# Kernel tuning notes

Measured on AMD Instinct MI355X. Metric: run time of the kernel, lower is better.

Reference implementation:

```python
import jax, jax.numpy as jnp
import numpy as np

B, L, D, H, DFF, C = 16, 1024, 256, 4, 2048, 3
NS, NC = 4, 4
DH = D // H


def _ln(x, g, b):
    m = x.mean(-1, keepdims=True)
    v = ((x - m) ** 2).mean(-1, keepdims=True)
    return (x - m) / jnp.sqrt(v + 1e-5) * g + b


def setup_inputs() -> dict:
    key = jax.random.key(0)
    ks = jax.random.split(key, 24)
    n = lambda k, s: jax.random.normal(k, s, jnp.float32) * 0.02
    return {
        'shape_idxs': jax.random.randint(ks[0], (B, L), 0, NS, jnp.int32),
        'color_idxs': jax.random.randint(ks[1], (B, L), 0, NC, jnp.int32),
        'shape_emb': n(ks[2], (NS, D)),
        'color_emb': n(ks[3], (NC, D)),
        'Wq': n(ks[4], (D, D)), 'bq': jnp.zeros((D,)),
        'Wk': n(ks[5], (D, D)), 'bk': jnp.zeros((D,)),
        'Wv': n(ks[6], (D, D)), 'bv': jnp.zeros((D,)),
        'Wo': n(ks[7], (D, D)), 'bo': jnp.zeros((D,)),
        'g1': jnp.ones((D,)), 'be1': jnp.zeros((D,)),
        'W1': n(ks[8], (D, DFF)), 'bf1': jnp.zeros((DFF,)),
        'W2': n(ks[9], (DFF, D)), 'bf2': jnp.zeros((D,)),
        'g2': jnp.ones((D,)), 'be2': jnp.zeros((D,)),
        'Wl': n(ks[10], (D, C)), 'bl': jnp.zeros((C,)),
        'Wp1': n(ks[11], (D, D)), 'bp1': jnp.zeros((D,)),
        'Wp2': n(ks[12], (D, 1)), 'bp2': jnp.zeros((1,)),
        'wc': n(ks[13], (1, 1)), 'bc': jnp.zeros((1,)),
    }


def reference(shape_idxs, color_idxs, shape_emb, color_emb, Wq, bq, Wk, bk, Wv, bv,
              Wo, bo, g1, be1, W1, bf1, W2, bf2, g2, be2, Wl, bl,
              Wp1, bp1, Wp2, bp2, wc, bc):
    # embed (dropout is identity in eval)
    x = shape_emb[shape_idxs] + color_emb[color_idxs]  # [B,L,D]
    # post-norm transformer encoder layer (PyTorch default)
    heads = lambda t: t.reshape(B, L, H, DH)
    q, k, v = heads(x @ Wq + bq), heads(x @ Wk + bk), heads(x @ Wv + bv)
    scores = jnp.einsum('blhd,bmhd->bhlm', q, k) / jnp.sqrt(jnp.float32(DH))
    attn = jax.nn.softmax(scores, axis=-1)
    ctx = jnp.einsum('bhlm,bmhd->blhd', attn, v).reshape(B, L, D)
    y = _ln(x + ctx @ Wo + bo, g1, be1)
    ff = jax.nn.relu(y @ W1 + bf1) @ W2 + bf2
    y = _ln(y + ff, g2, be2)  # trans_out [B,L,D]
    # latent logits / KL(prior || probs) with batchmean reduction
    logits = y @ Wl + bl
    logp = jax.nn.log_softmax(logits, axis=-1)
    prior = 1.0 / C
    kl_loss = jnp.sum(prior * (jnp.log(jnp.float32(prior)) - logp)) / B
    # data-dependent boundary segmentation (argmax of probs == argmax of logits)
    boundaries = (jnp.argmax(logits, axis=-1) == 0)
    boundaries = boundaries.at[:, 0].set(True)
    closed = boundaries & (jnp.arange(L) > 0)  # closure at l>0 ends segment at l
    seg_id = jnp.cumsum(closed.astype(jnp.int32), axis=1) - closed  # exclusive cumsum
    gid = (jnp.arange(B)[:, None] * L + seg_id).reshape(-1)  # global segment ids
    sums = jax.ops.segment_sum(y.reshape(B * L, D), gid, num_segments=B * L)
    counts = jax.ops.segment_sum(jnp.ones((B * L,), jnp.float32), gid, num_segments=B * L)
    means = sums / jnp.maximum(counts, 1.0)[:, None]  # per-segment mean [B*L,D]
    # predicate net + composition, mean over valid segments
    preds = jax.nn.sigmoid(jax.nn.relu(means @ Wp1 + bp1) @ Wp2 + bp2)  # [B*L,1]
    comp = (preds * wc[0, 0] + bc[0]).reshape(B, L)
    valid = (counts > 0).reshape(B, L).astype(jnp.float32)
    mean_comp = jnp.sum(comp * valid, axis=1) / jnp.sum(valid, axis=1)
    final_scores = jax.nn.sigmoid(mean_comp)
    return final_scores, kl_loss
```

## Files before the change

### kernel.cpp

```cpp
#include <hip/hip_runtime.h>


typedef unsigned short u16;
typedef u16    u16x4  __attribute__((ext_vector_type(4)));
typedef u16    u16x8  __attribute__((ext_vector_type(8)));
typedef __bf16 bf16x8 __attribute__((ext_vector_type(8)));
typedef float  f32x4  __attribute__((ext_vector_type(4)));

__device__ __forceinline__ float bf2f(u16 u) {
    union { unsigned int i; float f; } v; v.i = ((unsigned int)u) << 16; return v.f;
}
__device__ __forceinline__ u16 f2bf(float f) {
    union { float f; unsigned int i; } v; v.f = f;
    unsigned int r = (v.i + 0x7FFFu + ((v.i >> 16) & 1u)) >> 16;
    return (u16)r;
}
__device__ __forceinline__ u16 f2bf_fast(float f) {
    union { __bf16 h; u16 u; } v; v.h = (__bf16)f; return v.u;
}
__device__ __forceinline__ void gll16(const u16* g, u16* l) {
    __builtin_amdgcn_global_load_lds((__attribute__((address_space(1))) void*)(u16*)g,
                                     (__attribute__((address_space(3))) void*)l, 16, 0, 0);
}
__device__ __forceinline__ int get_mode(const int* __restrict__ detp) {
    int s = 0;
#pragma unroll 8
    for (int i = 0; i < 64; ++i) s += detp[i];
    return s > 16;
}

__global__ __launch_bounds__(256) void k_detect(const u16* __restrict__ w1raw,
                                                int* __restrict__ detp) {
    int i = blockIdx.x * 256 + threadIdx.x;
    int bad = 0;
    for (int k = i; k < 65536; k += 64 * 256) {
        unsigned v = w1raw[k] & 0x7FFFu;
        if (v >= 0x7F80u) bad++;
    }
    for (int off = 32; off >= 1; off >>= 1) bad += __shfl_xor(bad, off);
    __shared__ int bs[4];
    if ((threadIdx.x & 63) == 0) bs[threadIdx.x >> 6] = bad;
    __syncthreads();
    if (threadIdx.x == 0) detp[blockIdx.x] = bs[0] + bs[1] + bs[2] + bs[3];
}
__global__ void k_sentinel_f32(float* __restrict__ out, int code) {
    int t = threadIdx.x;
    if (t < 17) out[t] = (float)code;
}

struct PrepTab {
    const void* src[7];
    u16*        dst[7];
    int         K[7], N[7];
    float       scale[7];
    int         tstart[8];
    const void* isrc[17];
    unsigned    idstoff[17];
    int         in[17];
    float       iscale[17];
    u16*        ing;
};
__global__ __launch_bounds__(256) void k_prep(PrepTab tt, const int* __restrict__ detp) {
    int m = get_mode(detp);
    int bx = blockIdx.x;
    if (bx >= tt.tstart[7]) {
        int t = bx - tt.tstart[7];
        int n = tt.in[t];
        float sc = tt.iscale[t];
        u16* dst = tt.ing + tt.idstoff[t];
        for (int i = threadIdx.x; i < n; i += 256) {
            float v = m ? ((const float*)tt.isrc[t])[i] : bf2f(((const u16*)tt.isrc[t])[i]);
            dst[i] = f2bf(v * sc);
        }
        return;
    }
    __shared__ u16 tile[32][33];
    int wgt = 0;
#pragma unroll
    for (int i = 1; i < 7; ++i) if (bx >= tt.tstart[i]) wgt = i;
    int local = bx - tt.tstart[wgt];
    int K = tt.K[wgt], N = tt.N[wgt];
    float sc = tt.scale[wgt];
    int ntx = N >> 5;
    int txt = local % ntx, tyt = local / ntx;
    const void* W = tt.src[wgt];
    u16* Wt = tt.dst[wgt];
    int tx = threadIdx.x & 31, ty = threadIdx.x >> 5;
    int n = txt * 32 + tx;
    for (int i = ty; i < 32; i += 8) {
        size_t idx = (size_t)(tyt * 32 + i) * N + n;
        float v = m ? ((const float*)W)[idx] : bf2f(((const u16*)W)[idx]);
        tile[i][tx] = f2bf(v * sc);
    }
    __syncthreads();
    int k2 = tyt * 32 + tx;
    for (int i = ty; i < 32; i += 8) {
        int n2 = txt * 32 + i;
        Wt[(size_t)n2 * K + k2] = tile[tx][i];
    }
}

__global__ __launch_bounds__(256) void k_embed(const int* __restrict__ si,
                                               const int* __restrict__ ci,
                                               const void* __restrict__ se,
                                               const void* __restrict__ ce,
                                               u16* __restrict__ X,
                                               const int* __restrict__ detp) {
    int m = get_mode(detp);
    int t = blockIdx.x * 256 + threadIdx.x;
    int row = t >> 5, seg = (t & 31) * 8;
    int s = si[row], c = ci[row];
    u16x8 o;
    if (m) {
        const float* sp = (const float*)se + s * 256 + seg;
        const float* cp = (const float*)ce + c * 256 + seg;
#pragma unroll
        for (int e = 0; e < 8; ++e) o[e] = f2bf(sp[e] + cp[e]);
    } else {
        u16x8 a = *(const u16x8*)((const u16*)se + s * 256 + seg);
        u16x8 b = *(const u16x8*)((const u16*)ce + c * 256 + seg);
#pragma unroll
        for (int e = 0; e < 8; ++e) o[e] = f2bf(bf2f(a[e]) + bf2f(b[e]));
    }
    *(u16x8*)&X[(size_t)row * 256 + seg] = o;
}

__global__ __launch_bounds__(256) void k_gemm_bt(const u16* __restrict__ A,
                                                 const u16* __restrict__ Bt,
                                                 const u16* __restrict__ bias,
                                                 u16* __restrict__ C,
                                                 int N, int K, int relu, int gx) {
    __shared__ u16 As[128][32];
    __shared__ u16 Bs[128][32];
    const int tid = threadIdx.x;
    const int xcd = blockIdx.x & 7, j = blockIdx.x >> 3;
    const int m0 = (xcd * 16 + j / gx) * 128, n0 = (j % gx) * 128;
    const int lane = tid & 63, wid = tid >> 6;
    const int wm = (wid & 1) * 64, wn = (wid >> 1) * 64;
    const int m16 = lane & 15, quad = lane >> 4;
    f32x4 acc[4][4] = {};
    const int arow = tid >> 2;
    const int ac8  = (tid & 3) * 8;
    const u16* Ap0 = A  + (size_t)(m0 + arow) * K + ac8;
    const u16* Ap1 = A  + (size_t)(m0 + 64 + arow) * K + ac8;
    const u16* Bp0 = Bt + (size_t)(n0 + arow) * K + ac8;
    const u16* Bp1 = Bt + (size_t)(n0 + 64 + arow) * K + ac8;
    u16* lA0 = &As[arow][ac8];
    u16* lA1 = &As[64 + arow][ac8];
    u16* lB0 = &Bs[arow][ac8];
    u16* lB1 = &Bs[64 + arow][ac8];

    for (int k0 = 0; k0 < K; k0 += 32) {
        __syncthreads();
        gll16(Ap0 + k0, lA0);
        gll16(Ap1 + k0, lA1);
        gll16(Bp0 + k0, lB0);
        gll16(Bp1 + k0, lB1);
        __syncthreads();
        bf16x8 af[4], bfv[4];
#pragma unroll
        for (int i = 0; i < 4; ++i)
            af[i] = *(const bf16x8*)&As[wm + i * 16 + m16][quad * 8];
#pragma unroll
        for (int j2 = 0; j2 < 4; ++j2)
            bfv[j2] = *(const bf16x8*)&Bs[wn + j2 * 16 + m16][quad * 8];
#pragma unroll
        for (int i = 0; i < 4; ++i)
#pragma unroll
            for (int j2 = 0; j2 < 4; ++j2)
                acc[i][j2] = __builtin_amdgcn_mfma_f32_16x16x32_bf16(
                    af[i], bfv[j2], acc[i][j2], 0, 0, 0);
    }

#pragma unroll
    for (int i = 0; i < 4; ++i) {
        int row = m0 + wm + i * 16 + quad * 4;
#pragma unroll
        for (int j2 = 0; j2 < 4; ++j2) {
            int col = n0 + wn + j2 * 16 + m16;
            float bv = bf2f(bias[col]);
#pragma unroll
            for (int r = 0; r < 4; ++r) {
                float v = acc[i][j2][r] + bv;
                if (relu) v = fmaxf(v, 0.f);
                C[(size_t)(row + r) * N + col] = f2bf_fast(v);
            }
        }
    }
}

__global__ __launch_bounds__(256) void k_gemm64(const u16* __restrict__ A,
                                                const u16* __restrict__ Bt,
                                                const u16* __restrict__ bias,
                                                u16* __restrict__ C,
                                                int N, int K, int relu,
                                                int gx, int mtpx,
                                                u16* __restrict__ vt) {
    __shared__ u16 As0[64][32], As1[64][32];
    __shared__ u16 Bs0[128][32], Bs1[128][32];
    const int tid = threadIdx.x;
    const int xcd = blockIdx.x & 7, j = blockIdx.x >> 3;
    const int m0 = (xcd * mtpx + j / gx) * 64, n0 = (j % gx) * 128;
    const int vmode = (vt != nullptr) && (n0 >= 512);
    const int lane = tid & 63, wid = tid >> 6;
    const int wm = (wid & 1) * 32, wn = (wid >> 1) * 64;
    const int m16 = lane & 15, quad = lane >> 4;
    f32x4 acc[2][4] = {};
    const int arow = tid >> 2;
    const int ac8  = (tid & 3) * 8;
    const u16* Ap  = A  + (size_t)(m0 + arow) * K + ac8;
    const u16* Bp0 = Bt + (size_t)(n0 + arow) * K + ac8;
    const u16* Bp1 = Bt + (size_t)(n0 + 64 + arow) * K + ac8;
    u16* lA0  = &As0[arow][ac8];
    u16* lA1  = &As1[arow][ac8];
    u16* lB00 = &Bs0[arow][ac8];
    u16* lB01 = &Bs0[64 + arow][ac8];
    u16* lB10 = &Bs1[arow][ac8];
    u16* lB11 = &Bs1[64 + arow][ac8];

    for (int k0 = 0; k0 < K; k0 += 64) {
        __syncthreads();
        gll16(Ap + k0,        lA0);
        gll16(Ap + k0 + 32,   lA1);
        gll16(Bp0 + k0,       lB00);
        gll16(Bp0 + k0 + 32,  lB10);
        gll16(Bp1 + k0,       lB01);
        gll16(Bp1 + k0 + 32,  lB11);
        __syncthreads();
#pragma unroll
        for (int ks = 0; ks < 2; ++ks) {
            bf16x8 af[2], bfv[4];
#pragma unroll
            for (int i = 0; i < 2; ++i)
                af[i] = ks == 0 ? *(const bf16x8*)&As0[wm + i * 16 + m16][quad * 8]
                                : *(const bf16x8*)&As1[wm + i * 16 + m16][quad * 8];
#pragma unroll
            for (int j2 = 0; j2 < 4; ++j2)
                bfv[j2] = ks == 0 ? *(const bf16x8*)&Bs0[wn + j2 * 16 + m16][quad * 8]
                                  : *(const bf16x8*)&Bs1[wn + j2 * 16 + m16][quad * 8];
#pragma unroll
            for (int i = 0; i < 2; ++i)
#pragma unroll
                for (int j2 = 0; j2 < 4; ++j2)
                    acc[i][j2] = __builtin_amdgcn_mfma_f32_16x16x32_bf16(
                        af[i], bfv[j2], acc[i][j2], 0, 0, 0);
        }
    }

#pragma unroll
    for (int i = 0; i < 2; ++i) {
        int row = m0 + wm + i * 16 + quad * 4;
#pragma unroll
        for (int j2 = 0; j2 < 4; ++j2) {
            int col = n0 + wn + j2 * 16 + m16;
            float bv = bf2f(bias[col]);
            if (vmode) {
                int ch = col - 512;
                u16x4 o;
#pragma unroll
                for (int r = 0; r < 4; ++r) o[r] = f2bf_fast(acc[i][j2][r] + bv);
                size_t vb = ((size_t)((row >> 10) * 4 + (ch >> 6)) * 64 + (ch & 63)) * 1024
                          + (row & 1023);
                *(u16x4*)&vt[vb] = o;
            } else {
#pragma unroll
                for (int r = 0; r < 4; ++r) {
                    float v = acc[i][j2][r] + bv;
                    if (relu) v = fmaxf(v, 0.f);
                    C[(size_t)(row + r) * N + col] = f2bf_fast(v);
                }
            }
        }
    }
}

__global__ __launch_bounds__(256) void k_gemm64n(const u16* __restrict__ A,
                                                 const u16* __restrict__ Bt,
                                                 const u16* __restrict__ bias,
                                                 u16* __restrict__ C,
                                                 int N, int K, int relu,
                                                 int gnx, int mtpx,
                                                 const float* __restrict__ gate) {
    __shared__ u16 As0[64][32], As1[64][32];
    __shared__ u16 Bs0[64][32], Bs1[64][32];
    const int tid = threadIdx.x;
    const int xcd = blockIdx.x & 7, j = blockIdx.x >> 3;
    const int m0 = (xcd * mtpx + j / gnx) * 64, n0 = (j % gnx) * 64;
    if (gate && gate[m0] == 0.f) return;
    const int lane = tid & 63, w = tid >> 6;
    const int m16 = lane & 15, quad = lane >> 4;
    f32x4 acc[4] = {};
    const int arow = tid >> 2;
    const int ac8  = (tid & 3) * 8;
    const u16* Ap = A  + (size_t)(m0 + arow) * K + ac8;
    const u16* Bp = Bt + (size_t)(n0 + arow) * K + ac8;
    u16* lA0 = &As0[arow][ac8];
    u16* lA1 = &As1[arow][ac8];
    u16* lB0 = &Bs0[arow][ac8];
    u16* lB1 = &Bs1[arow][ac8];

    for (int k0 = 0; k0 < K; k0 += 64) {
        __syncthreads();
        gll16(Ap + k0,       lA0);
        gll16(Ap + k0 + 32,  lA1);
        gll16(Bp + k0,       lB0);
        gll16(Bp + k0 + 32,  lB1);
        __syncthreads();
#pragma unroll
        for (int ks = 0; ks < 2; ++ks) {
            bf16x8 af = ks == 0 ? *(const bf16x8*)&As0[w * 16 + m16][quad * 8]
                                : *(const bf16x8*)&As1[w * 16 + m16][quad * 8];
#pragma unroll
            for (int nt = 0; nt < 4; ++nt) {
                bf16x8 bfv = ks == 0 ? *(const bf16x8*)&Bs0[nt * 16 + m16][quad * 8]
                                     : *(const bf16x8*)&Bs1[nt * 16 + m16][quad * 8];
                acc[nt] = __builtin_amdgcn_mfma_f32_16x16x32_bf16(af, bfv, acc[nt], 0, 0, 0);
            }
        }
    }

#pragma unroll
    for (int nt = 0; nt < 4; ++nt) {
        int col = n0 + nt * 16 + m16;
        float bv = bf2f(bias[col]);
        int row = m0 + w * 16 + quad * 4;
#pragma unroll
        for (int r = 0; r < 4; ++r) {
            float v = acc[nt][r] + bv;
            if (relu) v = fmaxf(v, 0.f);
            C[(size_t)(row + r) * N + col] = f2bf_fast(v);
        }
    }
}

__global__ __launch_bounds__(256) void k_attn_mfma(const u16* __restrict__ QKV,
                                                   const u16* __restrict__ VT,
                                                   u16* __restrict__ CTX) {
    __shared__ u16 Ks[64][72];
    __shared__ u16 Vts[64][72];
    const int tid = threadIdx.x, lane = tid & 63, w = tid >> 6;
    const int quad = lane >> 4, c = lane & 15;
    const int blk = blockIdx.x;
    const int xcd = blk & 7, local = blk >> 3;
    const int bh = xcd * 8 + (local >> 4);
    const int qt = local & 15;
    const int b = bh >> 2, h = bh & 3;
    const int qrow0 = b * 1024 + qt * 64;

    const u16* qptr = QKV + (size_t)(qrow0 + w * 16 + c) * 768 + h * 64;
    bf16x8 aq0 = *(const bf16x8*)(qptr + quad * 8);
    bf16x8 aq1 = *(const bf16x8*)(qptr + 32 + quad * 8);

    bf16x8 ones;
    {
        union { u16 u; __bf16 h; } v; v.u = 0x3F80;
#pragma unroll
        for (int e = 0; e < 8; ++e) ones[e] = v.h;
    }

    f32x4 acc_o[4] = {};
    f32x4 acc_l = {};

    const u16* kbase  = QKV + (size_t)(b * 1024) * 768 + 256 + h * 64;
    const u16* vtbase = VT + (size_t)(bh * 64) * 1024;
    const int skk = tid >> 3, sc8 = (tid & 7) * 8;
    const int swk = (skk & ~12) | ((skk & 4) << 1) | ((skk & 8) >> 1);
    const int sra = ((c & 8) << 1) | (c & 4) | (c & 3);

    for (int t = 0; t < 16; ++t) {
        __syncthreads();
#pragma unroll
        for (int it = 0; it < 2; ++it) {
            int rr = skk + 32 * it;
            *(u16x8*)&Ks[swk + 32 * it][sc8] =
                *(const u16x8*)(kbase + (size_t)(t * 64 + rr) * 768 + sc8);
            *(u16x8*)&Vts[rr][sc8] = *(const u16x8*)(vtbase + (size_t)rr * 1024 + t * 64 + sc8);
        }
        __syncthreads();

#pragma unroll
        for (int ks = 0; ks < 2; ++ks) {
            const int ra = ks * 32 + sra;
            bf16x8 ka0 = *(const bf16x8*)&Ks[ra][quad * 8];
            bf16x8 ka1 = *(const bf16x8*)&Ks[ra][32 + quad * 8];
            bf16x8 kb0 = *(const bf16x8*)&Ks[ra + 8][quad * 8];
            bf16x8 kb1 = *(const bf16x8*)&Ks[ra + 8][32 + quad * 8];
            f32x4 za = {}, zb = {};
            za = __builtin_amdgcn_mfma_f32_16x16x32_bf16(ka0, aq0, za, 0, 0, 0);
            za = __builtin_amdgcn_mfma_f32_16x16x32_bf16(ka1, aq1, za, 0, 0, 0);
            zb = __builtin_amdgcn_mfma_f32_16x16x32_bf16(kb0, aq0, zb, 0, 0, 0);
            zb = __builtin_amdgcn_mfma_f32_16x16x32_bf16(kb1, aq1, zb, 0, 0, 0);

            bf16x8 ap;
#pragma unroll
            for (int r = 0; r < 4; ++r) {
                ap[r]     = (__bf16)exp2f(fminf(za[r], 80.f));
                ap[4 + r] = (__bf16)exp2f(fminf(zb[r], 80.f));
            }

            acc_l = __builtin_amdgcn_mfma_f32_16x16x32_bf16(ap, ones, acc_l, 0, 0, 0);
#pragma unroll
            for (int nt = 0; nt < 4; ++nt) {
                bf16x8 bv = *(const bf16x8*)&Vts[nt * 16 + c][ks * 32 + quad * 8];
                acc_o[nt] = __builtin_amdgcn_mfma_f32_16x16x32_bf16(ap, bv, acc_o[nt], 0, 0, 0);
            }
        }
    }

#pragma unroll
    for (int nt = 0; nt < 4; ++nt) {
        int col = h * 64 + nt * 16 + c;
#pragma unroll
        for (int r = 0; r < 4; ++r) {
            int row = qrow0 + w * 16 + quad * 4 + r;
            CTX[(size_t)row * 256 + col] = f2bf_fast(acc_o[nt][r] / acc_l[r]);
        }
    }
}

__global__ __launch_bounds__(256) void k_ln(const u16* __restrict__ A,
                                            const u16* __restrict__ R,
                                            const u16* __restrict__ g,
                                            const u16* __restrict__ be,
                                            u16* __restrict__ out) {
    int w = threadIdx.x >> 6, lane = threadIdx.x & 63;
    int row = blockIdx.x * 4 + w;
    size_t base = (size_t)row * 256 + lane * 4;
    u16x4 a4 = *(const u16x4*)&A[base];
    u16x4 r4 = *(const u16x4*)&R[base];
    float v[4];
    float s = 0.f, sq = 0.f;
#pragma unroll
    for (int j = 0; j < 4; ++j) {
        v[j] = bf2f(a4[j]) + bf2f(r4[j]);
        s += v[j]; sq += v[j] * v[j];
    }
    for (int off = 32; off >= 1; off >>= 1) { s += __shfl_xor(s, off); sq += __shfl_xor(sq, off); }
    float mean = s * (1.f / 256.f);
    float var  = sq * (1.f / 256.f) - mean * mean;
    float rs   = rsqrtf(var + 1e-5f);
    u16x4 o;
#pragma unroll
    for (int j = 0; j < 4; ++j) {
        int d = lane * 4 + j;
        o[j] = f2bf((v[j] - mean) * rs * bf2f(g[d]) + bf2f(be[d]));
    }
    *(u16x4*)&out[base] = o;
}

__global__ __launch_bounds__(256) void k_logits(const u16* __restrict__ FFO,
                                                const u16* __restrict__ Y1,
                                                const u16* __restrict__ g2,
                                                const u16* __restrict__ be2,
                                                const u16* __restrict__ Wl,
                                                const u16* __restrict__ bl,
                                                u16* __restrict__ Y2,
                                                float* __restrict__ klpart,
                                                int* __restrict__ flags) {
    const int tid = threadIdx.x, lane = tid & 63, w = tid >> 6;
    float wv[4][3], gv[4], bev[4];
#pragma unroll
    for (int j = 0; j < 4; ++j) {
        int d = lane * 4 + j;
        gv[j]  = bf2f(g2[d]);
        bev[j] = bf2f(be2[d]);
#pragma unroll
        for (int c = 0; c < 3; ++c) wv[j][c] = bf2f(Wl[d * 3 + c]);
    }
    const float b0 = bf2f(bl[0]), b1 = bf2f(bl[1]), b2 = bf2f(bl[2]);
    float klsum = 0.f;
    const int row0 = blockIdx.x * 16 + w * 4;
    for (int i = 0; i < 4; ++i) {
        int row = row0 + i;
        size_t base = (size_t)row * 256 + lane * 4;
        u16x4 f4 = *(const u16x4*)&FFO[base];
        u16x4 y4 = *(const u16x4*)&Y1[base];
        float v[4];
        float s = 0.f, sq = 0.f;
#pragma unroll
        for (int j = 0; j < 4; ++j) {
            v[j] = bf2f(f4[j]) + bf2f(y4[j]);
            s += v[j]; sq += v[j] * v[j];
        }
        for (int off = 32; off >= 1; off >>= 1) { s += __shfl_xor(s, off); sq += __shfl_xor(sq, off); }
        float mean = s * (1.f / 256.f);
        float var  = sq * (1.f / 256.f) - mean * mean;
        float rs   = rsqrtf(var + 1e-5f);
        u16x4 o;
        float a0 = 0.f, a1 = 0.f, a2 = 0.f;
#pragma unroll
        for (int j = 0; j < 4; ++j) {
            float yn = (v[j] - mean) * rs * gv[j] + bev[j];
            o[j] = f2bf(yn);
            float y = bf2f(o[j]);
            a0 += y * wv[j][0]; a1 += y * wv[j][1]; a2 += y * wv[j][2];
        }
        *(u16x4*)&Y2[base] = o;
        for (int off = 32; off >= 1; off >>= 1) {
            a0 += __shfl_xor(a0, off); a1 += __shfl_xor(a1, off); a2 += __shfl_xor(a2, off);
        }
        if (lane == 0) {
            float l0 = a0 + b0, l1 = a1 + b1, l2 = a2 + b2;
            float mx = fmaxf(l0, fmaxf(l1, l2));
            float lse = mx + __logf(__expf(l0 - mx) + __expf(l1 - mx) + __expf(l2 - mx));
            klsum += lse - (l0 + l1 + l2) * (1.f / 3.f) - 1.0986122886681098f;
            int am = 0; float bv = l0;
            if (l1 > bv) { bv = l1; am = 1; }
            if (l2 > bv) { am = 2; }
            int l = row & 1023;
            flags[row] = (am == 0 && l != 0) ? 1 : 0;
        }
    }
    __shared__ float kls[4];
    if (lane == 0) kls[w] = klsum;
    __syncthreads();
    if (tid == 0) klpart[blockIdx.x] = kls[0] + kls[1] + kls[2] + kls[3];
}

__global__ void k_scan(const int* __restrict__ flags, int* __restrict__ seg) {
    __shared__ int wsum[16];
    int b = blockIdx.x, t = threadIdx.x;
    int lane = t & 63, w = t >> 6;
    int f = flags[b * 1024 + t];
    int x = f;
#pragma unroll
    for (int off = 1; off < 64; off <<= 1) {
        int v = __shfl_up(x, off);
        if (lane >= off) x += v;
    }
    if (lane == 63) wsum[w] = x;
    __syncthreads();
    if (w == 0) {
        int s = (lane < 16) ? wsum[lane] : 0;
#pragma unroll
        for (int off = 1; off < 16; off <<= 1) {
            int v = __shfl_up(s, off);
            if (lane >= off) s += v;
        }
        if (lane < 16) wsum[lane] = s;
    }
    __syncthreads();
    int prefix = (w > 0) ? wsum[w - 1] : 0;
    seg[b * 1024 + t] = prefix + x - f;
}

__global__ __launch_bounds__(64) void k_segmean(const u16* __restrict__ Y,
                                                const int* __restrict__ seg,
                                                u16* __restrict__ means,
                                                float* __restrict__ cnt) {
    int g = blockIdx.x, lane = threadIdx.x;
    int b = g >> 10, s = g & 1023;
    const int* sb = seg + b * 1024;
    int target = s + (lane & 1);
    int lo = 0, hi = 1024;
    while (lo < hi) {
        int mid = (lo + hi) >> 1;
        if (sb[mid] < target) lo = mid + 1; else hi = mid;
    }
    int start = __shfl(lo, 0);
    int end   = __shfl(lo, 1);
    int n = end - start;
    if (lane == 0) cnt[g] = (float)n;
    if (n <= 0) return;
    f32x4 acc = {};
    for (int row = start; row < end; ++row) {
        u16x4 y4 = *(const u16x4*)&Y[(size_t)(b * 1024 + row) * 256 + lane * 4];
        acc[0] += bf2f(y4[0]); acc[1] += bf2f(y4[1]);
        acc[2] += bf2f(y4[2]); acc[3] += bf2f(y4[3]);
    }
    float inv = 1.f / (float)n;
    u16x4 o;
#pragma unroll
    for (int j = 0; j < 4; ++j) o[j] = f2bf(acc[j] * inv);
    *(u16x4*)&means[(size_t)g * 256 + lane * 4] = o;
}

__global__ __launch_bounds__(256) void k_preds(const u16* __restrict__ T,
                                               const u16* __restrict__ Wp2,
                                               const u16* __restrict__ bp2,
                                               const u16* __restrict__ wc,
                                               const u16* __restrict__ bc,
                                               const float* __restrict__ cnt,
                                               float* __restrict__ predp) {
    const int tid = threadIdx.x, lane = tid & 63, w = tid >> 6;
    float lwp[4];
#pragma unroll
    for (int j = 0; j < 4; ++j) lwp[j] = bf2f(Wp2[lane * 4 + j]);
    const float fb = bf2f(bp2[0]), fw = bf2f(wc[0]), fc = bf2f(bc[0]);
    float csum = 0.f, vsum = 0.f;
    const int g0 = blockIdx.x * 16 + w * 4;
    if (cnt[g0] != 0.f) {
        for (int i = 0; i < 4; ++i) {
            int g = g0 + i;
            u16x4 t4 = *(const u16x4*)&T[(size_t)g * 256 + lane * 4];
            float a = 0.f;
#pragma unroll
            for (int j = 0; j < 4; ++j) a += bf2f(t4[j]) * lwp[j];
            for (int off = 32; off >= 1; off >>= 1) a += __shfl_xor(a, off);
            if (lane == 0 && cnt[g] > 0.f) {
                float pred = 1.f / (1.f + __expf(-(a + fb)));
                csum += pred * fw + fc;
                vsum += 1.f;
            }
        }
    }
    __shared__ float cs[4], vs[4];
    if (lane == 0) { cs[w] = csum; vs[w] = vsum; }
    __syncthreads();
    if (tid == 0) {
        predp[2 * blockIdx.x]     = cs[0] + cs[1] + cs[2] + cs[3];
        predp[2 * blockIdx.x + 1] = vs[0] + vs[1] + vs[2] + vs[3];
    }
}

__global__ void k_final(const float* __restrict__ predp, const float* __restrict__ klp,
                        const int* __restrict__ detp, void* __restrict__ outv) {
    int t = threadIdx.x;
    float k = 0.f;
    for (int i = t; i < 1024; i += 64) k += klp[i];
    for (int off = 32; off >= 1; off >>= 1) k += __shfl_xor(k, off);
    float ktot = __shfl(k, 0);
    int batch = t >> 2, ch = t & 3;
    float c = 0.f, v = 0.f;
    for (int i = 0; i < 16; ++i) {
        int blk = batch * 64 + ch * 16 + i;
        c += predp[2 * blk];
        v += predp[2 * blk + 1];
    }
    c += __shfl_xor(c, 1); c += __shfl_xor(c, 2);
    v += __shfl_xor(v, 1); v += __shfl_xor(v, 2);
    int mode = get_mode(detp);
    if ((t & 3) == 0) {
        float d = v, nm = c;
        if (!(d > 0.f)) d = 1.f;
        if (isnan(nm) || isinf(nm)) nm = 0.f;
        float val = 1.f / (1.f + __expf(-nm / d));
        if (mode) ((float*)outv)[batch] = val;
        else      ((u16*)outv)[batch]   = f2bf(val);
    }
    if (t == 1) {
        float val = ktot * (1.f / 16.f);
        if (isnan(val) || isinf(val)) val = 0.f;
        if (mode) ((float*)outv)[16] = val;
        else      ((u16*)outv)[16]   = f2bf(val);
    }
}

extern "C" void kernel_launch(void* const* d_in, const int* in_sizes, int n_in,
                              void* d_out, int out_size, void* d_ws, size_t ws_size,
                              hipStream_t stream) {
    const int* shape_idxs = (const int*)d_in[0];
    const int* color_idxs = (const int*)d_in[1];
    char* ws = (char*)d_ws;
    const size_t MB = 1024 * 1024;

    if (ws_size < 90 * MB) {
        int wsMB = (int)(ws_size >> 20); if (wsMB > 250) wsMB = 250;
        k_sentinel_f32<<<1, 32, 0, stream>>>((float*)d_out, 200 + wsMB);
        return;
    }

    u16*   X     = (u16*)(ws);
    u16*   QKVb  = (u16*)(ws + 8 * MB);
    u16*   VT    = (u16*)(ws + 32 * MB);
    u16*   CTX   = (u16*)(ws + 40 * MB);
    u16*   CTXP  = (u16*)(ws + 48 * MB);
    u16*   Y1    = (u16*)(ws + 64 * MB);
    u16*   Hb    = (u16*)(ws);
    u16*   FFO   = (u16*)(ws + 72 * MB);
    u16*   Y2    = (u16*)(ws);
    u16*   MEANS = (u16*)(ws + 24 * MB);
    u16*   TB    = (u16*)(ws + 32 * MB);
    int*   FLAGS = (int*)(ws + 80 * MB);
    int*   SEG   = (int*)(ws + 80 * MB + 65536);
    float* CNT   = (float*)(ws + 80 * MB + 131072);
    float* KLP   = (float*)(ws + 80 * MB + 262144);
    float* PREDP = (float*)(ws + 80 * MB + 327680);
    u16*   W3T   = (u16*)(ws + 81 * MB);
    u16*   WoT   = (u16*)(ws + 81 * MB + 786432);
    u16*   Wp1T  = (u16*)(ws + 81 * MB + 917504);
    u16*   W1T   = (u16*)(ws + 82 * MB);
    u16*   W2T   = (u16*)(ws + 83 * MB);
    int*   DETP  = (int*)(ws + 84 * MB);
    u16*   ING   = (u16*)(ws + 85 * MB);

    const float QSCALE = 0.125f * 1.44269504f;

    PrepTab tt;
    const void* tsrc[7] = {d_in[4], d_in[6], d_in[8], d_in[10], d_in[22], d_in[14], d_in[16]};
    u16* tdst[7] = {W3T, W3T + 256 * 256, W3T + 512 * 256, WoT, Wp1T, W1T, W2T};
    int tK[7] = {256, 256, 256, 256, 256, 256, 2048};
    int tN[7] = {256, 256, 256, 256, 256, 2048, 256};
    int ts = 0;
    for (int i = 0; i < 7; ++i) {
        tt.src[i] = tsrc[i]; tt.dst[i] = tdst[i]; tt.K[i] = tK[i]; tt.N[i] = tN[i];
        tt.scale[i] = (i == 0) ? QSCALE : 1.0f;
        tt.tstart[i] = ts;
        ts += (tK[i] >> 5) * (tN[i] >> 5);
    }
    tt.tstart[7] = ts;

    static const int II[17]  = {5, 7, 9, 11, 12, 13, 15, 17, 18, 19, 20, 21, 23, 24, 25, 26, 27};
    static const int IN[17]  = {256, 256, 256, 256, 256, 256, 2048, 256, 256, 256, 768, 3, 256, 256, 1, 1, 1};
    unsigned off = 0;
    for (int i = 0; i < 17; ++i) {
        tt.isrc[i] = d_in[II[i]];
        tt.in[i] = IN[i];
        tt.iscale[i] = 1.0f;
        if (i == 0) { tt.idstoff[0] = off; off += 768; }
        else if (i == 1) tt.idstoff[1] = tt.idstoff[0] + 256;
        else if (i == 2) tt.idstoff[2] = tt.idstoff[0] + 512;
        else { tt.idstoff[i] = off; off += (unsigned)((IN[i] + 8) & ~7); }
    }
    tt.iscale[0] = QSCALE;
    tt.ing = ING;
    const u16* ib3  = ING + tt.idstoff[0];
    const u16* ibo  = ING + tt.idstoff[3];
    const u16* ig1  = ING + tt.idstoff[4];  const u16* ibe1 = ING + tt.idstoff[5];
    const u16* ibf1 = ING + tt.idstoff[6];  const u16* ibf2 = ING + tt.idstoff[7];
    const u16* ig2  = ING + tt.idstoff[8];  const u16* ibe2 = ING + tt.idstoff[9];
    const u16* iWl  = ING + tt.idstoff[10]; const u16* ibl  = ING + tt.idstoff[11];
    const u16* ibp1 = ING + tt.idstoff[12]; const u16* iWp2 = ING + tt.idstoff[13];
    const u16* ibp2 = ING + tt.idstoff[14]; const u16* iwc  = ING + tt.idstoff[15];
    const u16* ibc  = ING + tt.idstoff[16];

    k_detect<<<64, 256, 0, stream>>>((const u16*)d_in[14], DETP);
    k_prep<<<ts + 17, 256, 0, stream>>>(tt, DETP);
    k_embed<<<2048, 256, 0, stream>>>(shape_idxs, color_idxs, d_in[2], d_in[3], X, DETP);
    k_gemm64<<<1536, 256, 0, stream>>>(X, W3T, ib3, QKVb, 768, 256, 0, 6, 32, VT);
    k_attn_mfma<<<1024, 256, 0, stream>>>(QKVb, VT, CTX);
    k_gemm64n<<<1024, 256, 0, stream>>>(CTX, WoT, ibo, CTXP, 256, 256, 0, 4, 32, nullptr);
    k_ln<<<4096, 256, 0, stream>>>(CTXP, X, ig1, ibe1, Y1);
    k_gemm_bt<<<16 * 128, 256, 0, stream>>>(Y1, W1T, ibf1, Hb, 2048, 256, 1, 16);
    k_gemm64n<<<1024, 256, 0, stream>>>(Hb, W2T, ibf2, FFO, 256, 2048, 0, 4, 32, nullptr);
    k_logits<<<1024, 256, 0, stream>>>(FFO, Y1, ig2, ibe2, iWl, ibl, Y2, KLP, FLAGS);
    k_scan<<<16, 1024, 0, stream>>>(FLAGS, SEG);
    k_segmean<<<16384, 64, 0, stream>>>(Y2, SEG, MEANS, CNT);
    k_gemm64n<<<1024, 256, 0, stream>>>(MEANS, Wp1T, ibp1, TB, 256, 256, 1, 4, 32, CNT);
    k_preds<<<1024, 256, 0, stream>>>(TB, iWp2, ibp2, iwc, ibc, CNT, PREDP);
    k_final<<<1, 64, 0, stream>>>(PREDP, KLP, DETP, d_out);
}
```

Baseline: 301.1 us.

## Double-buffer K/V tiles in attention kernel with register prefetch

The attention kernel now keeps two LDS buffers for the K and V^T tiles. The next tile's global loads go into registers while the current tile is computed, then get stored into the other buffer. This hides global memory latency behind the MFMA and exp work and cuts the load-then-compute stall at each iteration. In exchange it doubles LDS use per block, which may lower occupancy, and it adds registers for the prefetched data.

```diff
diff --git a/kernel.cpp b/kernel.cpp
--- a/kernel.cpp
+++ b/kernel.cpp
@@ -336,8 +336,8 @@
 __global__ __launch_bounds__(256) void k_attn_mfma(const u16* __restrict__ QKV,
                                                    const u16* __restrict__ VT,
                                                    u16* __restrict__ CTX) {
-    __shared__ u16 Ks[64][72];
-    __shared__ u16 Vts[64][72];
+    __shared__ u16 Ks[2][64][72];
+    __shared__ u16 Vts[2][64][72];
     const int tid = threadIdx.x, lane = tid & 63, w = tid >> 6;
     const int quad = lane >> 4, c = lane & 15;
     const int blk = blockIdx.x;
@@ -367,45 +367,66 @@
     const int swk = (skk & ~12) | ((skk & 4) << 1) | ((skk & 8) >> 1);
     const int sra = ((c & 8) << 1) | (c & 4) | (c & 3);
 
-    for (int t = 0; t < 16; ++t) {
+    u16x8 rk0, rk1, rv0, rv1;
+
+#define LOADT(t) do {                                                          \
+    rk0 = *(const u16x8*)(kbase + (size_t)((t) * 64 + skk) * 768 + sc8);       \
+    rk1 = *(const u16x8*)(kbase + (size_t)((t) * 64 + skk + 32) * 768 + sc8);  \
+    rv0 = *(const u16x8*)(vtbase + (size_t)skk * 1024 + (t) * 64 + sc8);       \
+    rv1 = *(const u16x8*)(vtbase + (size_t)(skk + 32) * 1024 + (t) * 64 + sc8);\
+} while (0)
+
+#define STORET(bi) do {                                                        \
+    *(u16x8*)&Ks[bi][swk][sc8]       = rk0;                                    \
+    *(u16x8*)&Ks[bi][swk + 32][sc8]  = rk1;                                    \
+    *(u16x8*)&Vts[bi][skk][sc8]      = rv0;                                    \
+    *(u16x8*)&Vts[bi][skk + 32][sc8] = rv1;                                    \
+} while (0)
+
+#define COMPUTE(bi) do {                                                        \
+    _Pragma("unroll")                                                           \
+    for (int ks = 0; ks < 2; ++ks) {                                            \
+        const int ra = ks * 32 + sra;                                           \
+        bf16x8 ka0 = *(const bf16x8*)&Ks[bi][ra][quad * 8];                     \
+        bf16x8 ka1 = *(const bf16x8*)&Ks[bi][ra][32 + quad * 8];                \
+        bf16x8 kb0 = *(const bf16x8*)&Ks[bi][ra + 8][quad * 8];                 \
+        bf16x8 kb1 = *(const bf16x8*)&Ks[bi][ra + 8][32 + quad * 8];            \
+        f32x4 za = {}, zb = {};                                                 \
+        za = __builtin_amdgcn_mfma_f32_16x16x32_bf16(ka0, aq0, za, 0, 0, 0);    \
+        za = __builtin_amdgcn_mfma_f32_16x16x32_bf16(ka1, aq1, za, 0, 0, 0);    \
+        zb = __builtin_amdgcn_mfma_f32_16x16x32_bf16(kb0, aq0, zb, 0, 0, 0);    \
+        zb = __builtin_amdgcn_mfma_f32_16x16x32_bf16(kb1, aq1, zb, 0, 0, 0);    \
+        bf16x8 ap;                                                              \
+        _Pragma("unroll")                                                       \
+        for (int r = 0; r < 4; ++r) {                                           \
+            ap[r]     = (__bf16)exp2f(fminf(za[r], 80.f));                      \
+            ap[4 + r] = (__bf16)exp2f(fminf(zb[r], 80.f));                      \
+        }                                                                       \
+        acc_l = __builtin_amdgcn_mfma_f32_16x16x32_bf16(ap, ones, acc_l, 0, 0, 0);\
+        _Pragma("unroll")                                                       \
+        for (int nt = 0; nt < 4; ++nt) {                                        \
+            bf16x8 bv = *(const bf16x8*)&Vts[bi][nt * 16 + c][ks * 32 + quad * 8];\
+            acc_o[nt] = __builtin_amdgcn_mfma_f32_16x16x32_bf16(ap, bv, acc_o[nt], 0, 0, 0);\
+        }                                                                       \
+    }                                                                           \
+} while (0)
+
+    LOADT(0);
+    STORET(0);
+    for (int t = 0; t < 16; t += 2) {
         __syncthreads();
-#pragma unroll
-        for (int it = 0; it < 2; ++it) {
-            int rr = skk + 32 * it;
-            *(u16x8*)&Ks[swk + 32 * it][sc8] =
-                *(const u16x8*)(kbase + (size_t)(t * 64 + rr) * 768 + sc8);
-            *(u16x8*)&Vts[rr][sc8] = *(const u16x8*)(vtbase + (size_t)rr * 1024 + t * 64 + sc8);
-        }
+        LOADT(t + 1);
+        COMPUTE(0);
+        STORET(1);
         __syncthreads();
-
-#pragma unroll
-        for (int ks = 0; ks < 2; ++ks) {
-            const int ra = ks * 32 + sra;
-            bf16x8 ka0 = *(const bf16x8*)&Ks[ra][quad * 8];
-            bf16x8 ka1 = *(const bf16x8*)&Ks[ra][32 + quad * 8];
-            bf16x8 kb0 = *(const bf16x8*)&Ks[ra + 8][quad * 8];
-            bf16x8 kb1 = *(const bf16x8*)&Ks[ra + 8][32 + quad * 8];
-            f32x4 za = {}, zb = {};
-            za = __builtin_amdgcn_mfma_f32_16x16x32_bf16(ka0, aq0, za, 0, 0, 0);
-            za = __builtin_amdgcn_mfma_f32_16x16x32_bf16(ka1, aq1, za, 0, 0, 0);
-            zb = __builtin_amdgcn_mfma_f32_16x16x32_bf16(kb0, aq0, zb, 0, 0, 0);
-            zb = __builtin_amdgcn_mfma_f32_16x16x32_bf16(kb1, aq1, zb, 0, 0, 0);
-
-            bf16x8 ap;
-#pragma unroll
-            for (int r = 0; r < 4; ++r) {
-                ap[r]     = (__bf16)exp2f(fminf(za[r], 80.f));
-                ap[4 + r] = (__bf16)exp2f(fminf(zb[r], 80.f));
-            }
-
-            acc_l = __builtin_amdgcn_mfma_f32_16x16x32_bf16(ap, ones, acc_l, 0, 0, 0);
-#pragma unroll
-            for (int nt = 0; nt < 4; ++nt) {
-                bf16x8 bv = *(const bf16x8*)&Vts[nt * 16 + c][ks * 32 + quad * 8];
-                acc_o[nt] = __builtin_amdgcn_mfma_f32_16x16x32_bf16(ap, bv, acc_o[nt], 0, 0, 0);
-            }
-        }
-    }
+        if (t + 2 < 16) LOADT(t + 2);
+        COMPUTE(1);
+        if (t + 2 < 16) STORET(0);
+    }
+
+#undef LOADT
+#undef STORET
+#undef COMPUTE
 
 #pragma unroll
     for (int nt = 0; nt < 4; ++nt) {
```

Result: faster. 289.3 us (-3.9%).
